# Optimization experiments

Measured on AMD Instinct MI355X. Metric: run time of the kernel, lower is better.

The kernel has to match this reference:

```python
import jax, jax.numpy as jnp
import numpy as np

D_MODEL = 1024
NUM_HEADS = 16
NUM_KV_HEADS = 4
HEAD_DIM = D_MODEL // NUM_HEADS  # 64
THETA = 10000.0
MAX_SEQ_LEN = 4096


def _rope_tables(max_seq_len, d_k, theta):
    k_vec = jnp.arange(0, d_k, 2, dtype=jnp.float32) / d_k
    freq = 1.0 / (theta ** k_vec)                       # (d_k/2,)
    ang = jnp.arange(max_seq_len, dtype=jnp.float32)[:, None] * freq[None, :]
    return jnp.cos(ang), jnp.sin(ang)                   # each (max_seq_len, d_k/2)


def _apply_rope(x, pos, cos_table, sin_table):
    # x: (b, h, l, d), pos: (b, l)
    cos = cos_table[pos][:, None, :, :]                 # (b, 1, l, d/2)
    sin = sin_table[pos][:, None, :, :]
    even, odd = x[..., 0::2], x[..., 1::2]
    r1 = even * cos - odd * sin
    r2 = even * sin + odd * cos
    return jnp.stack([r1, r2], axis=-1).reshape(x.shape)  # interleave back


def setup_inputs() -> dict:
    key = jax.random.key(0)
    ks = jax.random.split(key, 6)
    B, L, D = 1, 4096, D_MODEL
    std = (2.0 / (D + D)) ** 0.5
    std_kv = (2.0 / (D + HEAD_DIM * NUM_KV_HEADS)) ** 0.5
    x = jax.random.normal(ks[0], (B, L, D), dtype=jnp.float32)
    Wq = jax.random.normal(ks[1], (D, D), dtype=jnp.float32) * std
    Wk = jax.random.normal(ks[2], (HEAD_DIM * NUM_KV_HEADS, D), dtype=jnp.float32) * std_kv
    Wv = jax.random.normal(ks[3], (HEAD_DIM * NUM_KV_HEADS, D), dtype=jnp.float32) * std_kv
    Wo = jax.random.normal(ks[4], (D, D), dtype=jnp.float32) * std
    token_positions = jnp.broadcast_to(jnp.arange(L, dtype=jnp.int32), (B, L))
    return {"x": x, "Wq": Wq, "Wk": Wk, "Wv": Wv, "Wo": Wo,
            "token_positions": token_positions}


def reference(x, Wq, Wk, Wv, Wo, token_positions):
    B, L, D = x.shape
    H, Hkv, Dh = NUM_HEADS, NUM_KV_HEADS, HEAD_DIM
    n_rep = H // Hkv
    cos_t, sin_t = _rope_tables(MAX_SEQ_LEN, Dh, THETA)

    q = (x @ Wq.T).reshape(B, L, H, Dh).transpose(0, 2, 1, 3)      # b h l d
    k = (x @ Wk.T).reshape(B, L, Hkv, Dh).transpose(0, 2, 1, 3)    # b g l d
    v = (x @ Wv.T).reshape(B, L, Hkv, Dh).transpose(0, 2, 1, 3)

    q = _apply_rope(q, token_positions, cos_t, sin_t)
    k = _apply_rope(k, token_positions, cos_t, sin_t)

    # GQA: group query heads by kv head
    qg = q.reshape(B, Hkv, n_rep, L, Dh)
    scores = jnp.einsum('bgrqd,bgkd->bgrqk', qg, k) / jnp.sqrt(jnp.float32(Dh))
    causal = jnp.tril(jnp.ones((L, L), dtype=bool))
    scores = jnp.where(causal, scores, -jnp.inf)
    weights = jax.nn.softmax(scores, axis=-1)
    out = jnp.einsum('bgrqk,bgkd->bgrqd', weights, v)              # b g r q d
    out = out.reshape(B, H, L, Dh).transpose(0, 2, 1, 3).reshape(B, L, D)
    return out @ Wo.T
```

## Files before the change

kernel.cpp:

```cpp
#include <hip/hip_runtime.h>
#include <hip/hip_bf16.h>
#include <math.h>

typedef __bf16 bf16;
typedef __bf16 v8bf __attribute__((ext_vector_type(8)));
typedef __bf16 v4bf __attribute__((ext_vector_type(4)));
typedef __bf16 v2bf __attribute__((ext_vector_type(2)));
typedef float f32x4 __attribute__((ext_vector_type(4)));
typedef float f32x16 __attribute__((ext_vector_type(16)));

#define L_SEQ 4096
#define DMODEL 1024
#define NHEADS 16
#define DH 64
#define NEG_BIG (-1e30f)
#define LN1E4_64 0.14391156f
#define SCL2 0.18033688f
#define DEFER_THR 8.0f

static __device__ __forceinline__ unsigned pkbf(float x, float y) {
    v2bf t; t[0] = (bf16)x; t[1] = (bf16)y;
    return __builtin_bit_cast(unsigned, t);
}

static __device__ __forceinline__ void gld16(const bf16* g, const bf16* l) {
    __builtin_amdgcn_global_load_lds((const __attribute__((address_space(1))) void*)g,
                                     (__attribute__((address_space(3))) void*)l, 16, 0, 0);
}

__global__ void convert_all(const float* __restrict__ x, const float* __restrict__ wq,
                            const float* __restrict__ wk, const float* __restrict__ wv,
                            const float* __restrict__ wo,
                            bf16* __restrict__ xb, bf16* __restrict__ wqkvb,
                            bf16* __restrict__ wob) {
    int i = (blockIdx.x * 256 + threadIdx.x) * 4;
    const float* src;
    bf16* dst;
    if (i < 4194304)      { src = x  + i;             dst = xb    + i; }
    else if (i < 5242880) { src = wq + (i - 4194304); dst = wqkvb + (i - 4194304); }
    else if (i < 5505024) { src = wk + (i - 5242880); dst = wqkvb + 1048576 + (i - 5242880); }
    else if (i < 5767168) { src = wv + (i - 5505024); dst = wqkvb + 1310720 + (i - 5505024); }
    else                  { src = wo + (i - 5767168); dst = wob   + (i - 5767168); }
    f32x4 v = *(const f32x4*)src;
    v4bf r;
#pragma unroll
    for (int j = 0; j < 4; j++) r[j] = (bf16)v[j];
    *(v4bf*)dst = r;
}

__global__ __launch_bounds__(512) void gemm_qkv(const bf16* __restrict__ A,
                                                const bf16* __restrict__ W,
                                                bf16* __restrict__ Qb,
                                                bf16* __restrict__ Kb,
                                                bf16* __restrict__ Vtg,
                                                const int* __restrict__ tp) {
    __shared__ bf16 As[2][128][64];
    __shared__ bf16 Bs[2][128][64];
    const int K = 1024;
    const int tid = threadIdx.x;
    const int w = tid >> 6, lane = tid & 63;
    const int quad = lane >> 4, l16 = lane & 15;
    const int wm = (w & 1) * 64, wn = (w >> 1) * 32;
    const int bm = blockIdx.x * 128, bn = blockIdx.y * 128;

    const int srow = lane >> 3;
    const int scol = ((lane & 7) ^ srow) << 3;

    f32x4 acc[4][2];
#pragma unroll
    for (int mf = 0; mf < 4; mf++)
#pragma unroll
        for (int nf = 0; nf < 2; nf++) acc[mf][nf] = (f32x4){0.f, 0.f, 0.f, 0.f};

#define QKV_STAGE(buf, ktt)                                                        \
    do {                                                                           \
        const bf16* ga = &A[(size_t)(bm + (w << 3) + srow) * 1024 + (ktt) + scol]; \
        const bf16* gb = &W[(size_t)(bn + (w << 3) + srow) * 1024 + (ktt) + scol]; \
        gld16(ga,             &As[buf][(w << 3)][0]);                              \
        gld16(ga + 64 * 1024, &As[buf][64 + (w << 3)][0]);                         \
        gld16(gb,             &Bs[buf][(w << 3)][0]);                              \
        gld16(gb + 64 * 1024, &Bs[buf][64 + (w << 3)][0]);                         \
    } while (0)

    QKV_STAGE(0, 0);
    __syncthreads();

    int cur = 0;
    for (int kt = 0; kt < K; kt += 64) {
        const bool more = (kt + 64) < K;
        if (more) QKV_STAGE(cur ^ 1, kt + 64);
#pragma unroll
        for (int kf = 0; kf < 2; kf++) {
            v8bf a[4], b[2];
#pragma unroll
            for (int mf = 0; mf < 4; mf++)
                a[mf] = *(v8bf*)&As[cur][wm + mf * 16 + l16][(((kf << 2) + quad) ^ (l16 & 7)) << 3];
#pragma unroll
            for (int nf = 0; nf < 2; nf++)
                b[nf] = *(v8bf*)&Bs[cur][wn + nf * 16 + l16][(((kf << 2) + quad) ^ (l16 & 7)) << 3];
#pragma unroll
            for (int mf = 0; mf < 4; mf++)
#pragma unroll
                for (int nf = 0; nf < 2; nf++)
                    acc[mf][nf] = __builtin_amdgcn_mfma_f32_16x16x32_bf16(a[mf], b[nf], acc[mf][nf], 0, 0, 0);
        }
        __syncthreads();
        cur ^= 1;
    }
#undef QKV_STAGE

    if (bn < 1024) {
#pragma unroll
        for (int mf = 0; mf < 4; mf++) {
            int pos_[4];
#pragma unroll
            for (int r = 0; r < 4; r++) pos_[r] = tp[bm + wm + mf * 16 + quad * 4 + r];
#pragma unroll
            for (int nf = 0; nf < 2; nf++) {
                const int col = bn + wn + nf * 16 + l16;
                float fr = __expf(-(float)((col & 63) & ~1) * LN1E4_64);
#pragma unroll
                for (int r = 0; r < 4; r++) {
                    float v = acc[mf][nf][r];
                    float sn, cs;
                    __sincosf((float)pos_[r] * fr, &sn, &cs);
                    float p = __shfl_xor(v, 1);
                    float res = (l16 & 1) ? (p * sn + v * cs) : (v * cs - p * sn);
                    int row = bm + wm + mf * 16 + quad * 4 + r;
                    Qb[(size_t)row * DMODEL + col] = (bf16)(res * SCL2);
                }
            }
        }
    } else if (bn < 1280) {
#pragma unroll
        for (int mf = 0; mf < 4; mf++) {
            int pos_[4];
#pragma unroll
            for (int r = 0; r < 4; r++) pos_[r] = tp[bm + wm + mf * 16 + quad * 4 + r];
#pragma unroll
            for (int nf = 0; nf < 2; nf++) {
                const int kcol = bn - 1024 + wn + nf * 16 + l16;
                float fr = __expf(-(float)((kcol & 63) & ~1) * LN1E4_64);
#pragma unroll
                for (int r = 0; r < 4; r++) {
                    float v = acc[mf][nf][r];
                    float sn, cs;
                    __sincosf((float)pos_[r] * fr, &sn, &cs);
                    float p = __shfl_xor(v, 1);
                    float res = (l16 & 1) ? (p * sn + v * cs) : (v * cs - p * sn);
                    int row = bm + wm + mf * 16 + quad * 4 + r;
                    Kb[(size_t)row * 256 + kcol] = (bf16)res;
                }
            }
        }
    } else {
#pragma unroll
        for (int mf = 0; mf < 4; mf++)
#pragma unroll
            for (int nf = 0; nf < 2; nf++) {
                v4bf pk;
#pragma unroll
                for (int r = 0; r < 4; r++) pk[r] = (bf16)acc[mf][nf][r];
                int vcol = bn - 1280 + wn + nf * 16 + l16;
                int row = bm + wm + mf * 16 + quad * 4;
                *(v4bf*)&Vtg[(size_t)vcol * L_SEQ + row] = pk;
            }
    }
}

__global__ __launch_bounds__(512) void gemm_out(const bf16* __restrict__ A,
                                                const bf16* __restrict__ W,
                                                float* __restrict__ C) {
    __shared__ bf16 As[2][128][64];
    __shared__ bf16 Bs[2][128][64];
    const int K = 1024, N = 1024;
    const int tid = threadIdx.x;
    const int w = tid >> 6, lane = tid & 63;
    const int quad = lane >> 4, l16 = lane & 15;
    const int wm = (w & 1) * 64, wn = (w >> 1) * 32;
    const int bm = blockIdx.x * 128, bn = blockIdx.y * 128;

    const int srow = lane >> 3;
    const int scol = ((lane & 7) ^ srow) << 3;

    f32x4 acc[4][2];
#pragma unroll
    for (int mf = 0; mf < 4; mf++)
#pragma unroll
        for (int nf = 0; nf < 2; nf++) acc[mf][nf] = (f32x4){0.f, 0.f, 0.f, 0.f};

#define OUT_STAGE(buf, ktt)                                                        \
    do {                                                                           \
        const bf16* ga = &A[(size_t)(bm + (w << 3) + srow) * 1024 + (ktt) + scol]; \
        const bf16* gb = &W[(size_t)(bn + (w << 3) + srow) * 1024 + (ktt) + scol]; \
        gld16(ga,             &As[buf][(w << 3)][0]);                              \
        gld16(ga + 64 * 1024, &As[buf][64 + (w << 3)][0]);                         \
        gld16(gb,             &Bs[buf][(w << 3)][0]);                              \
        gld16(gb + 64 * 1024, &Bs[buf][64 + (w << 3)][0]);                         \
    } while (0)

    OUT_STAGE(0, 0);
    __syncthreads();

    int cur = 0;
    for (int kt = 0; kt < K; kt += 64) {
        const bool more = (kt + 64) < K;
        if (more) OUT_STAGE(cur ^ 1, kt + 64);
#pragma unroll
        for (int kf = 0; kf < 2; kf++) {
            v8bf a[4], b[2];
#pragma unroll
            for (int mf = 0; mf < 4; mf++)
                a[mf] = *(v8bf*)&As[cur][wm + mf * 16 + l16][(((kf << 2) + quad) ^ (l16 & 7)) << 3];
#pragma unroll
            for (int nf = 0; nf < 2; nf++)
                b[nf] = *(v8bf*)&Bs[cur][wn + nf * 16 + l16][(((kf << 2) + quad) ^ (l16 & 7)) << 3];
#pragma unroll
            for (int mf = 0; mf < 4; mf++)
#pragma unroll
                for (int nf = 0; nf < 2; nf++)
                    acc[mf][nf] = __builtin_amdgcn_mfma_f32_16x16x32_bf16(a[mf], b[nf], acc[mf][nf], 0, 0, 0);
        }
        __syncthreads();
        cur ^= 1;
    }
#undef OUT_STAGE

#pragma unroll
    for (int mf = 0; mf < 4; mf++)
#pragma unroll
        for (int nf = 0; nf < 2; nf++)
#pragma unroll
            for (int r = 0; r < 4; r++) {
                int row = bm + wm + mf * 16 + quad * 4 + r;
                int col = bn + wn + nf * 16 + l16;
                C[(size_t)row * N + col] = acc[mf][nf][r];
            }
}

__global__ __launch_bounds__(256, 2) void flash12(const bf16* __restrict__ Q,
                                                  const bf16* __restrict__ Kb,
                                                  const bf16* __restrict__ Vtg,
                                                  bf16* __restrict__ O0,
                                                  bf16* __restrict__ O1,
                                                  float* __restrict__ ML) {
    __shared__ bf16 Ks[128][68];
    __shared__ bf16 Vt[64][132];
    const int h = blockIdx.x, kvh = h >> 2;
    const int i = blockIdx.y;
    const int qb = 31 - (i >> 1);
    const int half = i & 1;
    const int tid = threadIdx.x;
    const int w = tid >> 6, lane = tid & 63;
    const int l32 = lane & 31, hi = lane >> 5;
    const int krow = tid >> 1, kcb = (tid & 1) * 32;
    const int vr = tid >> 2, vcb = (tid & 3) * 32;

    const int T = qb + 1;
    const int k0 = half ? ((T + 1) >> 1) : 0;
    const int k1 = half ? T : ((T + 1) >> 1);
    bf16* Op = half ? O1 : O0;
    float* mlp = ML + (size_t)(half * NHEADS + h) * L_SEQ * 2;

    if (k0 >= k1) {
        for (int ii = tid; ii < 128 * 64; ii += 256) {
            int rr = ii >> 6, cc = ii & 63;
            Op[(size_t)(qb * 128 + rr) * DMODEL + h * DH + cc] = (bf16)0.f;
        }
        if (tid < 128) {
            mlp[(qb * 128 + tid) * 2 + 0] = NEG_BIG;
            mlp[(qb * 128 + tid) * 2 + 1] = 0.f;
        }
        return;
    }

    v8bf ones;
#pragma unroll
    for (int j = 0; j < 8; j++) ones[j] = (bf16)1.0f;

    const int qrow = qb * 128 + w * 32 + l32;
    v8bf qf[4];
#pragma unroll
    for (int d16 = 0; d16 < 4; d16++)
        qf[d16] = *(const v8bf*)&Q[(size_t)qrow * DMODEL + h * DH + d16 * 16 + hi * 8];

    f32x16 oaccT[2], lacc;
#pragma unroll
    for (int d = 0; d < 2; d++)
#pragma unroll
        for (int r = 0; r < 16; r++) oaccT[d][r] = 0.f;
#pragma unroll
    for (int r = 0; r < 16; r++) lacc[r] = 0.f;
    float m_i = NEG_BIG;

    v8bf kreg[4], vreg[4];
    {
        const bf16* ks = &Kb[(size_t)(k0 * 128 + krow) * 256 + kvh * DH + kcb];
        const bf16* vs = &Vtg[(size_t)(kvh * DH + vr) * L_SEQ + k0 * 128 + vcb];
#pragma unroll
        for (int u = 0; u < 4; u++) { kreg[u] = *(const v8bf*)&ks[8 * u]; vreg[u] = *(const v8bf*)&vs[8 * u]; }
#pragma unroll
        for (int u = 0; u < 4; u++) { *(v8bf*)&Ks[krow][kcb + 8 * u] = kreg[u]; *(v8bf*)&Vt[vr][vcb + 8 * u] = vreg[u]; }
    }

    for (int kb = k0; kb < k1; kb++) {
        __syncthreads();
        if (kb + 1 < k1) {
            const bf16* ks = &Kb[(size_t)((kb + 1) * 128 + krow) * 256 + kvh * DH + kcb];
            const bf16* vs = &Vtg[(size_t)(kvh * DH + vr) * L_SEQ + (kb + 1) * 128 + vcb];
#pragma unroll
            for (int u = 0; u < 4; u++) { kreg[u] = *(const v8bf*)&ks[8 * u]; vreg[u] = *(const v8bf*)&vs[8 * u]; }
        }

        f32x16 s[4];
        __builtin_amdgcn_s_setprio(1);
#pragma unroll
        for (int n = 0; n < 4; n++) {
#pragma unroll
            for (int r = 0; r < 16; r++) s[n][r] = 0.f;
#pragma unroll
            for (int d16 = 0; d16 < 4; d16++) {
                v8bf av = *(v8bf*)&Ks[n * 32 + l32][d16 * 16 + hi * 8];
                s[n] = __builtin_amdgcn_mfma_f32_32x32x16_bf16(av, qf[d16], s[n], 0, 0, 0);
            }
        }
        __builtin_amdgcn_s_setprio(0);

        if (kb == qb) {
#pragma unroll
            for (int n = 0; n < 4; n++) {
                int kbase = kb * 128 + n * 32 + 4 * hi;
#pragma unroll
                for (int r = 0; r < 16; r++) {
                    int key = kbase + (r & 3) + 8 * (r >> 2);
                    if (key > qrow) s[n][r] = NEG_BIG;
                }
            }
        }

        float mx = NEG_BIG;
#pragma unroll
        for (int n = 0; n < 4; n++)
#pragma unroll
            for (int r = 0; r < 16; r += 2)
                mx = fmaxf(fmaxf(mx, s[n][r]), s[n][r + 1]);
        mx = fmaxf(mx, __shfl_xor(mx, 32));

        if (!__all(mx <= m_i + DEFER_THR)) {
            float mnew = fmaxf(m_i, mx);
            float alpha = exp2f(m_i - mnew);
#pragma unroll
            for (int r = 0; r < 16; r++) lacc[r] *= alpha;
#pragma unroll
            for (int d = 0; d < 2; d++)
#pragma unroll
                for (int r = 0; r < 16; r++) oaccT[d][r] *= alpha;
            m_i = mnew;
        }

#pragma unroll
        for (int n = 0; n < 4; n++)
#pragma unroll
            for (int r = 0; r < 16; r++)
                s[n][r] = exp2f(s[n][r] - m_i);

        __builtin_amdgcn_s_setprio(1);
#pragma unroll
        for (int n = 0; n < 4; n++) {
#pragma unroll
            for (int u = 0; u < 2; u++) {
                const int ro = u * 8;
                unsigned a0 = pkbf(s[n][ro + 0], s[n][ro + 1]);
                unsigned a1 = pkbf(s[n][ro + 2], s[n][ro + 3]);
                unsigned b0 = pkbf(s[n][ro + 4], s[n][ro + 5]);
                unsigned b1 = pkbf(s[n][ro + 6], s[n][ro + 7]);
#if __has_builtin(__builtin_amdgcn_permlane32_swap)
                auto s0 = __builtin_amdgcn_permlane32_swap(a0, b0, false, false);
                auto s1 = __builtin_amdgcn_permlane32_swap(a1, b1, false, false);
                unsigned w0 = s0[0], w2 = s0[1], w1 = s1[0], w3 = s1[1];
#else
                unsigned t0 = hi ? a0 : b0;
                unsigned r0 = __shfl_xor(t0, 32);
                unsigned w0 = hi ? r0 : a0, w2 = hi ? b0 : r0;
                unsigned t1 = hi ? a1 : b1;
                unsigned r1 = __shfl_xor(t1, 32);
                unsigned w1 = hi ? r1 : a1, w3 = hi ? b1 : r1;
#endif
                union { unsigned uu[4]; v8bf v; } pf;
                pf.uu[0] = w0; pf.uu[1] = w1; pf.uu[2] = w2; pf.uu[3] = w3;
                const int t = n * 2 + u;
#pragma unroll
                for (int dblk = 0; dblk < 2; dblk++) {
                    v8bf av = *(v8bf*)&Vt[dblk * 32 + l32][t * 16 + hi * 8];
                    oaccT[dblk] = __builtin_amdgcn_mfma_f32_32x32x16_bf16(av, pf.v, oaccT[dblk], 0, 0, 0);
                }
                lacc = __builtin_amdgcn_mfma_f32_32x32x16_bf16(ones, pf.v, lacc, 0, 0, 0);
            }
        }
        __builtin_amdgcn_s_setprio(0);

        __syncthreads();
        if (kb + 1 < k1) {
#pragma unroll
            for (int u = 0; u < 4; u++) { *(v8bf*)&Ks[krow][kcb + 8 * u] = kreg[u]; *(v8bf*)&Vt[vr][vcb + 8 * u] = vreg[u]; }
        }
    }

    __syncthreads();
#pragma unroll
    for (int dblk = 0; dblk < 2; dblk++)
#pragma unroll
        for (int r = 0; r < 16; r++) {
            int d = dblk * 32 + (r & 3) + 8 * (r >> 2) + 4 * hi;
            Ks[w * 32 + l32][d] = (bf16)oaccT[dblk][r];
        }
    asm volatile("s_waitcnt lgkmcnt(0)" ::: "memory");
    __builtin_amdgcn_sched_barrier(0);
#pragma unroll
    for (int ii = 0; ii < 4; ii++) {
        int cc = (lane & 1) * 32 + ii * 8;
        int rr = w * 32 + (lane >> 1);
        v8bf ov = *(v8bf*)&Ks[rr][cc];
        *(v8bf*)&Op[(size_t)(qb * 128 + rr) * DMODEL + h * DH + cc] = ov;
    }
    if (hi == 0) {
        mlp[qrow * 2 + 0] = m_i;
        mlp[qrow * 2 + 1] = lacc[0];
    }
}

__global__ void combine(const bf16* __restrict__ O0, const bf16* __restrict__ O1,
                        const float* __restrict__ ML, bf16* __restrict__ Attn) {
    int gid = blockIdx.x * 256 + threadIdx.x;
    int row = gid >> 8;
    int cg = (gid & 255) * 4;
    int h = cg >> 6;
    const float* ml0 = ML + ((size_t)h * L_SEQ + row) * 2;
    const float* ml1 = ML + ((size_t)(NHEADS + h) * L_SEQ + row) * 2;
    float m0 = ml0[0], l0 = ml0[1], m1 = ml1[0], l1 = ml1[1];
    float m = fmaxf(m0, m1);
    float a0 = exp2f(m0 - m), a1 = exp2f(m1 - m);
    float inv = 1.f / (a0 * l0 + a1 * l1);
    v4bf o0 = *(const v4bf*)&O0[(size_t)row * DMODEL + cg];
    v4bf o1 = *(const v4bf*)&O1[(size_t)row * DMODEL + cg];
    v4bf res;
#pragma unroll
    for (int j = 0; j < 4; j++)
        res[j] = (bf16)((a0 * (float)o0[j] + a1 * (float)o1[j]) * inv);
    *(v4bf*)&Attn[(size_t)row * DMODEL + cg] = res;
}

extern "C" void kernel_launch(void* const* d_in, const int* in_sizes, int n_in,
                              void* d_out, int out_size, void* d_ws, size_t ws_size,
                              hipStream_t stream) {
    const float* x  = (const float*)d_in[0];
    const float* Wq = (const float*)d_in[1];
    const float* Wk = (const float*)d_in[2];
    const float* Wv = (const float*)d_in[3];
    const float* Wo = (const float*)d_in[4];
    const int*   tp = (const int*)d_in[5];
    float* out = (float*)d_out;

    bf16*  xb    = (bf16*)d_ws;
    bf16*  wqkvb = xb    + 4194304;
    bf16*  wob   = wqkvb + 1572864;
    bf16*  Qb    = wob   + 1048576;
    bf16*  Kb    = Qb    + 4194304;
    bf16*  Vtg   = Kb    + 1048576;
    float* MLf   = (float*)(Vtg + 1048576);
    bf16*  Attn  = xb;
    bf16*  O0    = (bf16*)d_out;
    bf16*  O1    = O0 + 4194304;

    convert_all<<<6656, 256, 0, stream>>>(x, Wq, Wk, Wv, Wo, xb, wqkvb, wob);
    gemm_qkv<<<dim3(32, 12), 512, 0, stream>>>(xb, wqkvb, Qb, Kb, Vtg, tp);
    flash12<<<dim3(NHEADS, 64), 256, 0, stream>>>(Qb, Kb, Vtg, O0, O1, MLf);
    combine<<<4096, 256, 0, stream>>>(O0, O1, MLf, Attn);
    gemm_out<<<dim3(32, 8), 512, 0, stream>>>(Attn, wob, out);
}
```

Measured before the change: 192.2 us.

## Use 256-row query tiles with 512 threads and balanced key-range split

```diff
diff --git a/kernel.cpp b/kernel.cpp
--- a/kernel.cpp
+++ b/kernel.cpp
@@ -238,7 +238,7 @@
             }
 }
 
-__global__ __launch_bounds__(256, 2) void flash12(const bf16* __restrict__ Q,
+__global__ __launch_bounds__(512, 2) void flash13(const bf16* __restrict__ Q,
                                                   const bf16* __restrict__ Kb,
                                                   const bf16* __restrict__ Vtg,
                                                   bf16* __restrict__ O0,
@@ -248,37 +248,24 @@
     __shared__ bf16 Vt[64][132];
     const int h = blockIdx.x, kvh = h >> 2;
     const int i = blockIdx.y;
-    const int qb = 31 - (i >> 1);
-    const int half = i & 1;
+    const int qb = (i < 16) ? (15 - (i >> 1)) : ((i - 16) >> 1);
+    const int z = i & 1;
     const int tid = threadIdx.x;
     const int w = tid >> 6, lane = tid & 63;
     const int l32 = lane & 31, hi = lane >> 5;
-    const int krow = tid >> 1, kcb = (tid & 1) * 32;
-    const int vr = tid >> 2, vcb = (tid & 3) * 32;
-
-    const int T = qb + 1;
-    const int k0 = half ? ((T + 1) >> 1) : 0;
-    const int k1 = half ? T : ((T + 1) >> 1);
-    bf16* Op = half ? O1 : O0;
-    float* mlp = ML + (size_t)(half * NHEADS + h) * L_SEQ * 2;
-
-    if (k0 >= k1) {
-        for (int ii = tid; ii < 128 * 64; ii += 256) {
-            int rr = ii >> 6, cc = ii & 63;
-            Op[(size_t)(qb * 128 + rr) * DMODEL + h * DH + cc] = (bf16)0.f;
-        }
-        if (tid < 128) {
-            mlp[(qb * 128 + tid) * 2 + 0] = NEG_BIG;
-            mlp[(qb * 128 + tid) * 2 + 1] = 0.f;
-        }
-        return;
-    }
+    const int krow = tid >> 2, kcb = (tid & 3) * 16;
+    const int vr = tid >> 3, vcb = (tid & 7) * 16;
+
+    const int k0 = z ? (qb + 1) : 0;
+    const int k1 = z ? (2 * qb + 2) : (qb + 1);
+    bf16* Op = z ? O1 : O0;
+    float* mlp = ML + (size_t)(z * NHEADS + h) * L_SEQ * 2;
 
     v8bf ones;
 #pragma unroll
     for (int j = 0; j < 8; j++) ones[j] = (bf16)1.0f;
 
-    const int qrow = qb * 128 + w * 32 + l32;
+    const int qrow = qb * 256 + w * 32 + l32;
     v8bf qf[4];
 #pragma unroll
     for (int d16 = 0; d16 < 4; d16++)
@@ -293,14 +280,14 @@
     for (int r = 0; r < 16; r++) lacc[r] = 0.f;
     float m_i = NEG_BIG;
 
-    v8bf kreg[4], vreg[4];
+    v8bf kreg[2], vreg[2];
     {
         const bf16* ks = &Kb[(size_t)(k0 * 128 + krow) * 256 + kvh * DH + kcb];
         const bf16* vs = &Vtg[(size_t)(kvh * DH + vr) * L_SEQ + k0 * 128 + vcb];
-#pragma unroll
-        for (int u = 0; u < 4; u++) { kreg[u] = *(const v8bf*)&ks[8 * u]; vreg[u] = *(const v8bf*)&vs[8 * u]; }
-#pragma unroll
-        for (int u = 0; u < 4; u++) { *(v8bf*)&Ks[krow][kcb + 8 * u] = kreg[u]; *(v8bf*)&Vt[vr][vcb + 8 * u] = vreg[u]; }
+        kreg[0] = *(const v8bf*)ks; kreg[1] = *(const v8bf*)(ks + 8);
+        vreg[0] = *(const v8bf*)vs; vreg[1] = *(const v8bf*)(vs + 8);
+        *(v8bf*)&Ks[krow][kcb] = kreg[0]; *(v8bf*)&Ks[krow][kcb + 8] = kreg[1];
+        *(v8bf*)&Vt[vr][vcb] = vreg[0];   *(v8bf*)&Vt[vr][vcb + 8] = vreg[1];
     }
 
     for (int kb = k0; kb < k1; kb++) {
@@ -308,8 +295,8 @@
         if (kb + 1 < k1) {
             const bf16* ks = &Kb[(size_t)((kb + 1) * 128 + krow) * 256 + kvh * DH + kcb];
             const bf16* vs = &Vtg[(size_t)(kvh * DH + vr) * L_SEQ + (kb + 1) * 128 + vcb];
-#pragma unroll
-            for (int u = 0; u < 4; u++) { kreg[u] = *(const v8bf*)&ks[8 * u]; vreg[u] = *(const v8bf*)&vs[8 * u]; }
+            kreg[0] = *(const v8bf*)ks; kreg[1] = *(const v8bf*)(ks + 8);
+            vreg[0] = *(const v8bf*)vs; vreg[1] = *(const v8bf*)(vs + 8);
         }
 
         f32x16 s[4];
@@ -326,7 +313,7 @@
         }
         __builtin_amdgcn_s_setprio(0);
 
-        if (kb == qb) {
+        if (kb >= 2 * qb) {
 #pragma unroll
             for (int n = 0; n < 4; n++) {
                 int kbase = kb * 128 + n * 32 + 4 * hi;
@@ -401,31 +388,38 @@
 
         __syncthreads();
         if (kb + 1 < k1) {
-#pragma unroll
-            for (int u = 0; u < 4; u++) { *(v8bf*)&Ks[krow][kcb + 8 * u] = kreg[u]; *(v8bf*)&Vt[vr][vcb + 8 * u] = vreg[u]; }
-        }
-    }
-
-    __syncthreads();
-#pragma unroll
-    for (int dblk = 0; dblk < 2; dblk++)
-#pragma unroll
-        for (int r = 0; r < 16; r++) {
-            int d = dblk * 32 + (r & 3) + 8 * (r >> 2) + 4 * hi;
-            Ks[w * 32 + l32][d] = (bf16)oaccT[dblk][r];
-        }
-    asm volatile("s_waitcnt lgkmcnt(0)" ::: "memory");
-    __builtin_amdgcn_sched_barrier(0);
-#pragma unroll
-    for (int ii = 0; ii < 4; ii++) {
-        int cc = (lane & 1) * 32 + ii * 8;
-        int rr = w * 32 + (lane >> 1);
-        v8bf ov = *(v8bf*)&Ks[rr][cc];
-        *(v8bf*)&Op[(size_t)(qb * 128 + rr) * DMODEL + h * DH + cc] = ov;
-    }
+            *(v8bf*)&Ks[krow][kcb] = kreg[0]; *(v8bf*)&Ks[krow][kcb + 8] = kreg[1];
+            *(v8bf*)&Vt[vr][vcb] = vreg[0];   *(v8bf*)&Vt[vr][vcb + 8] = vreg[1];
+        }
+    }
+
     if (hi == 0) {
         mlp[qrow * 2 + 0] = m_i;
         mlp[qrow * 2 + 1] = lacc[0];
+    }
+
+#pragma unroll
+    for (int ph = 0; ph < 2; ph++) {
+        __syncthreads();
+        if ((w >> 2) == ph) {
+            const int wr = (w & 3) * 32 + l32;
+#pragma unroll
+            for (int dblk = 0; dblk < 2; dblk++)
+#pragma unroll
+                for (int r = 0; r < 16; r++) {
+                    int d = dblk * 32 + (r & 3) + 8 * (r >> 2) + 4 * hi;
+                    Ks[wr][d] = (bf16)oaccT[dblk][r];
+                }
+        }
+        __syncthreads();
+        {
+            const int rr = tid >> 2, cc = (tid & 3) * 16;
+            const int row = qb * 256 + ph * 128 + rr;
+            v8bf ov0 = *(v8bf*)&Ks[rr][cc];
+            v8bf ov1 = *(v8bf*)&Ks[rr][cc + 8];
+            *(v8bf*)&Op[(size_t)row * DMODEL + h * DH + cc] = ov0;
+            *(v8bf*)&Op[(size_t)row * DMODEL + h * DH + cc + 8] = ov1;
+        }
     }
 }
 
@@ -474,7 +468,7 @@
 
     convert_all<<<6656, 256, 0, stream>>>(x, Wq, Wk, Wv, Wo, xb, wqkvb, wob);
     gemm_qkv<<<dim3(32, 12), 512, 0, stream>>>(xb, wqkvb, Qb, Kb, Vtg, tp);
-    flash12<<<dim3(NHEADS, 64), 256, 0, stream>>>(Qb, Kb, Vtg, O0, O1, MLf);
+    flash13<<<dim3(NHEADS, 32), 512, 0, stream>>>(Qb, Kb, Vtg, O0, O1, MLf);
     combine<<<4096, 256, 0, stream>>>(O0, O1, MLf, Attn);
     gemm_out<<<dim3(32, 8), 512, 0, stream>>>(Attn, wob, out);
 }
```

Measured after the change: 210.7 us. 1.1x slower.
